# Optimization experiments

Measured on AMD Instinct MI355X. Metric: run time of the kernel, lower is better.

## Reference

```python
import jax, jax.numpy as jnp
import numpy as np

N, V_DIM, P_DIM, Q_DIM, C_DIM, H_DIM = 1536, 128, 16, 16, 16, 32
N_MOL, N_EDGE, LAYERS = 64, 16384, 3
TAU, GAMMA = 0.2, 1.0


def setup_inputs() -> dict:
    key = jax.random.key(0)
    ks = jax.random.split(key, 16)
    rng = np.random.default_rng(0)

    v_features = jax.random.normal(ks[0], (N, V_DIM), dtype=jnp.float32)

    # molecule -> node assignment: 64 molecules x 24 nodes each (block structure)
    mol_id = np.repeat(np.arange(N_MOL), N // N_MOL)
    mnm = np.zeros((N_MOL, N), dtype=np.float32)
    mnm[mol_id, np.arange(N)] = 1.0
    mol_node_mask = (mnm - 1.0) * 1e9  # 0 where assigned, -1e9 otherwise

    # node-edge incidence matrix [N, E]
    src = rng.integers(0, N, N_EDGE)
    dst = rng.integers(0, N, N_EDGE)
    nem = np.zeros((N, N_EDGE), dtype=np.float32)
    nem[src, np.arange(N_EDGE)] = 1.0
    nem[dst, np.arange(N_EDGE)] = 1.0
    node_edge_mask = np.zeros((N, N_EDGE), dtype=np.float32)

    def lin(k, fan_in, fan_out):
        kw, kb = jax.random.split(k)
        s = 1.0 / np.sqrt(fan_in)
        W = jax.random.uniform(kw, (fan_in, fan_out), jnp.float32, -s, s)
        b = jax.random.uniform(kb, (fan_out,), jnp.float32, -s, s)
        return W, b

    Wp, bp = lin(ks[1], V_DIM, P_DIM)
    Wq, bq = lin(ks[2], V_DIM, Q_DIM)
    Wc, bc = lin(ks[3], Q_DIM, C_DIM)
    W1, b1 = lin(ks[4], P_DIM + Q_DIM + C_DIM, H_DIM)
    Wdp, bdp = lin(ks[5], H_DIM, P_DIM)
    Wdq, bdq = lin(ks[6], H_DIM, Q_DIM)
    Wa, ba = lin(ks[7], P_DIM + Q_DIM, 1)

    return dict(v_features=v_features,
                mol_node_matrix=jnp.asarray(mnm), mol_node_mask=jnp.asarray(mol_node_mask),
                node_edge_matrix=jnp.asarray(nem), node_edge_mask=jnp.asarray(node_edge_mask),
                Wp=Wp, bp=bp, Wq=Wq, bq=bq, Wc=Wc, bc=bc,
                W1=W1, b1=b1, Wdp=Wdp, bdp=bdp, Wdq=Wdq, bdq=bdq, Wa=Wa, ba=ba)


def _safe_pair_norm(q):
    # pairwise ||q_i - q_j|| with grad-safe sqrt (zero diag)
    sq = ((q[None, :, :] - q[:, None, :]) ** 2).sum(-1)  # [N,N]
    return jnp.where(sq > 0, jnp.sqrt(jnp.where(sq > 0, sq, 1.0)), 0.0)


def reference(v_features, mol_node_matrix, mol_node_mask, node_edge_matrix, node_edge_mask,
              Wp, bp, Wq, bq, Wc, bc, W1, b1, Wdp, bdp, Wdq, bdq, Wa, ba):
    n = v_features.shape[0]
    m = mol_node_matrix.T @ mol_node_matrix                      # [N,N] same-molecule mask
    e = node_edge_matrix @ node_edge_matrix.T                    # [N,N] adjacency counts
    e = e * (1.0 - jnp.eye(n, dtype=e.dtype))                    # zero diagonal

    p = v_features @ Wp + bp                                     # [N,p]
    q = v_features @ Wq + bq                                     # [N,q]
    c_loss = jnp.linalg.norm(mol_node_matrix @ q)

    for _ in range(LAYERS):
        diff = q[None, :, :] - q[:, None, :]                     # [N,N,q]
        cenc = diff @ Wc + bc                                    # [N,N,c]  (large intermediate, as in torch)
        c = jnp.einsum('ij,ijc->ic', m, cenc)                    # masked sum over j
        h = jax.nn.relu(jnp.concatenate([p, q, c], axis=1) @ W1 + b1)
        dp = jnp.tanh(h @ Wdp + bdp)
        dq = jnp.tanh(h @ Wdq + bdq)
        p = p + TAU * dp
        q = q + TAU * dq
        c_loss = c_loss + jnp.linalg.norm(mol_node_matrix @ q)

    x = jnp.concatenate([p, q], axis=1)                          # [N, p+q]
    w = (x @ Wa + ba)[:, 0]                                      # [N]
    att = jax.nn.softmax(mol_node_matrix * w[None, :] + mol_node_mask, axis=1)  # [n_mol, N]
    f = att @ x                                                  # [n_mol, p+q]

    s_loss = jnp.abs(p).sum()
    a_loss = (e * jax.nn.relu(_safe_pair_norm(q) - GAMMA)).sum()
    return (f, s_loss, c_loss, a_loss)
```

## Files before the change

### kernel.cpp

```cpp
#include <hip/hip_runtime.h>
#include <hip/hip_bf16.h>
#include <math.h>

#define N_NODES 1536
#define V_DIMC  128
#define NMOL    64
#define NEDGE   16384
#define MAXM    24
#define SCANB   2048
#define TAU     0.2f

__device__ __forceinline__ float ldv(const void* p, int i, bool b16) {
    if (b16) {
        unsigned int u = ((unsigned int)((const unsigned short*)p)[i]) << 16;
        float f; __builtin_memcpy(&f, &u, 4); return f;
    }
    return ((const float*)p)[i];
}
__device__ __forceinline__ void stv(void* p, int i, float v, bool b16) {
    if (b16) ((__hip_bfloat16*)p)[i] = __float2bfloat16(v);
    else     ((float*)p)[i] = v;
}

__global__ __launch_bounds__(256) void k_init(const void* __restrict__ mnm,
        int* __restrict__ flag, int* __restrict__ cnt) {
    int t = blockIdx.x * 256 + threadIdx.x;
    if (t < NEDGE) cnt[t] = 0;
    if (t == 0) {
        unsigned int w = *(const unsigned int*)mnm;
        *flag = (w == 0x3F800000u) ? 0 : 1;
    }
}

__global__ __launch_bounds__(384) void k_mega(
        const void* __restrict__ mnm, const void* __restrict__ nem,
        const void* __restrict__ v,
        const void* __restrict__ Wp, const void* __restrict__ bp,
        const void* __restrict__ Wq, const void* __restrict__ bq,
        const void* __restrict__ Wc, const void* __restrict__ bc,
        const void* __restrict__ W1, const void* __restrict__ b1,
        const void* __restrict__ Wdp, const void* __restrict__ bdp,
        const void* __restrict__ Wdq, const void* __restrict__ bdq,
        const void* __restrict__ Wa, const void* __restrict__ ba,
        const int* __restrict__ flag, int* __restrict__ cnt, int* __restrict__ srow,
        float* __restrict__ qg, float* __restrict__ s_part,
        float* __restrict__ c_part, void* __restrict__ out) {
    __shared__ int   mi[MAXM];
    __shared__ float mw[MAXM];
    __shared__ int   nmem_s;
    __shared__ float rs_s, ba_s, inv_s;
    __shared__ float Wp_l[V_DIMC * 16], Wq_l[V_DIMC * 16];
    __shared__ float Wc_l[256], W1_l[48 * 32], Wdp_l[512], Wdq_l[512];
    __shared__ float bp_l[16], bq_l[16], bc_l[16], b1_l[32], bdp_l[16], bdq_l[16], Wa_l[32];
    __shared__ float P[MAXM][17], Q[MAXM][17], XQ[MAXM][17], XC[MAXM][17], H[MAXM][33];
    __shared__ float msum[16], wv[MAXM], attw[MAXM];
    __shared__ float red[512];

    const bool b16 = flag[0] != 0;
    const int t = threadIdx.x;

    if (blockIdx.x >= NMOL) {
        int sb = blockIdx.x - NMOL;
        const int stride = SCANB * 384;
        if (b16) {
            const int total8 = N_NODES * NEDGE / 8;
            const uint4* src = (const uint4*)nem;
            for (int i = sb * 384 + t; i < total8; i += stride) {
                uint4 x = src[i];
                if ((x.x | x.y | x.z | x.w) == 0u) continue;
                int base = i * 8, row = base >> 14, k0 = base & (NEDGE - 1);
                unsigned int wd[4] = {x.x, x.y, x.z, x.w};
                for (int w2 = 0; w2 < 4; ++w2) {
                    unsigned int ww = wd[w2];
                    if (!ww) continue;
                    if (ww & 0xFFFFu) { int k = k0 + 2 * w2;     int s = atomicAdd(&cnt[k], 1); if (s < 2) srow[k * 2 + s] = row; }
                    if (ww >> 16)     { int k = k0 + 2 * w2 + 1; int s = atomicAdd(&cnt[k], 1); if (s < 2) srow[k * 2 + s] = row; }
                }
            }
        } else {
            const int total4 = N_NODES * NEDGE / 4;
            const float4* src = (const float4*)nem;
            for (int i = sb * 384 + t; i < total4; i += stride) {
                float4 x = src[i];
                if (x.x == 0.f && x.y == 0.f && x.z == 0.f && x.w == 0.f) continue;
                int base = i * 4, row = base >> 14, k0 = base & (NEDGE - 1);
                float vv[4] = {x.x, x.y, x.z, x.w};
                for (int u = 0; u < 4; ++u) if (vv[u] != 0.f) {
                    int k = k0 + u; int s = atomicAdd(&cnt[k], 1); if (s < 2) srow[k * 2 + s] = row;
                }
            }
        }
        return;
    }

    const int g = blockIdx.x;

    for (int i = t; i < V_DIMC * 16; i += 384) { Wp_l[i] = ldv(Wp, i, b16); Wq_l[i] = ldv(Wq, i, b16); }
    for (int i = t; i < 48 * 32; i += 384) W1_l[i] = ldv(W1, i, b16);
    for (int i = t; i < 512; i += 384) { Wdp_l[i] = ldv(Wdp, i, b16); Wdq_l[i] = ldv(Wdq, i, b16); }
    if (t < 256) Wc_l[t] = ldv(Wc, t, b16);
    if (t < 16) { bp_l[t] = ldv(bp, t, b16); bq_l[t] = ldv(bq, t, b16); bc_l[t] = ldv(bc, t, b16);
                  bdp_l[t] = ldv(bdp, t, b16); bdq_l[t] = ldv(bdq, t, b16); }
    if (t < 32) { b1_l[t] = ldv(b1, t, b16); Wa_l[t] = ldv(Wa, t, b16); }
    if (t < MAXM) { mi[t] = 0; mw[t] = 0.f; }
    if (t == 0) ba_s = ldv(ba, 0, b16);

    if (t < 64) {
        int lane = t, base = 0;
        for (int r = 0; r < N_NODES / 64; ++r) {
            float w = ldv(mnm, g * N_NODES + r * 64 + lane, b16);
            unsigned long long bm = __ballot(w != 0.f);
            if (w != 0.f) {
                int pos = base + __popcll(bm & ((1ull << lane) - 1ull));
                if (pos < MAXM) { mi[pos] = r * 64 + lane; mw[pos] = w; }
            }
            base += __popcll(bm);
        }
        if (lane == 0) {
            nmem_s = (base > MAXM) ? MAXM : base;
            float s = 0.f;
            for (int m2 = 0; m2 < nmem_s; ++m2) s += mw[m2];
            rs_s = s;
        }
    }
    __syncthreads();
    const int nm = nmem_s;
    const int m = t >> 4, d = t & 15;
    const float rs = rs_s;

    if (m < nm) {
        int node = mi[m];
        float accp = bp_l[d], accq = bq_l[d];
        for (int e = 0; e < V_DIMC; ++e) {
            float vv = ldv(v, node * V_DIMC + e, b16);
            accp += vv * Wp_l[e * 16 + d];
            accq += vv * Wq_l[e * 16 + d];
        }
        P[m][d] = accp; Q[m][d] = accq;
    }

    for (int layer = 0; layer < 4; ++layer) {
        __syncthreads();
        if (t < 16) {
            float s = 0.f;
            for (int m2 = 0; m2 < nm; ++m2) s += mw[m2] * Q[m2][t];
            msum[t] = s;
        }
        __syncthreads();
        if (t == 0) {
            float ss = 0.f;
            for (int e = 0; e < 16; ++e) ss += msum[e] * msum[e];
            c_part[layer * NMOL + g] = ss;
        }
        if (layer == 3) break;
        float pi = 0.f, qi = 0.f;
        if (m < nm) {
            pi = P[m][d]; qi = Q[m][d];
            XQ[m][d] = mw[m] * (msum[d] - rs * qi);
        }
        __syncthreads();
        if (m < nm) {
            float c = mw[m] * rs * bc_l[d];
            for (int e = 0; e < 16; ++e) c += XQ[m][e] * Wc_l[e * 16 + d];
            XC[m][d] = c;
        }
        __syncthreads();
        if (m < nm) {
            float h0 = b1_l[d], h1 = b1_l[16 + d];
            for (int e = 0; e < 48; ++e) {
                float xv = (e < 16) ? P[m][e] : (e < 32) ? Q[m][e - 16] : XC[m][e - 32];
                h0 += xv * W1_l[e * 32 + d];
                h1 += xv * W1_l[e * 32 + 16 + d];
            }
            H[m][d] = fmaxf(h0, 0.f); H[m][16 + d] = fmaxf(h1, 0.f);
        }
        __syncthreads();
        if (m < nm) {
            float dp = bdp_l[d], dq = bdq_l[d];
            for (int e = 0; e < 32; ++e) {
                float hv = H[m][e];
                dp += hv * Wdp_l[e * 16 + d];
                dq += hv * Wdq_l[e * 16 + d];
            }
            P[m][d] = pi + TAU * tanhf(dp);
            Q[m][d] = qi + TAU * tanhf(dq);
        }
    }
    __syncthreads();

    if (m < nm) qg[mi[m] * 16 + d] = Q[m][d];

    red[t] = (m < nm) ? fabsf(P[m][d]) : 0.f;
    if (t < 128) red[384 + t] = 0.f;
    __syncthreads();
    for (int s = 256; s > 0; s >>= 1) { if (t < s) red[t] += red[t + s]; __syncthreads(); }
    if (t == 0) s_part[g] = red[0];

    if (t < nm) {
        float acc = ba_s;
        for (int e = 0; e < 16; ++e) acc += P[t][e] * Wa_l[e] + Q[t][e] * Wa_l[16 + e];
        wv[t] = acc;
    }
    __syncthreads();
    if (t == 0) {
        float mx = -3.0e38f;
        for (int m2 = 0; m2 < nm; ++m2) mx = fmaxf(mx, wv[m2]);
        float s = 0.f;
        for (int m2 = 0; m2 < nm; ++m2) { float ex = expf(wv[m2] - mx); attw[m2] = ex; s += ex; }
        inv_s = 1.f / s;
    }
    __syncthreads();
    if (t < 32) {
        float acc = 0.f;
        for (int m2 = 0; m2 < nm; ++m2)
            acc += attw[m2] * ((t < 16) ? P[m2][t] : Q[m2][t - 16]);
        stv(out, g * 32 + t, acc * inv_s, b16);
    }
}

__global__ __launch_bounds__(256) void k_aloss(const int* __restrict__ cnt,
        const int* __restrict__ srow, const float* __restrict__ qg,
        float* __restrict__ apart) {
    __shared__ float red[256];
    int t = threadIdx.x;
    int k = blockIdx.x * 256 + t;
    float local = 0.f;
    if (cnt[k] == 2) {
        int ia = srow[k * 2], ib = srow[k * 2 + 1];
        if (ia != ib) {
            float d2 = 0.f;
            for (int e = 0; e < 16; ++e) {
                float df = qg[ia * 16 + e] - qg[ib * 16 + e];
                d2 += df * df;
            }
            if (d2 > 0.f) {
                float r = sqrtf(d2) - 1.0f;
                if (r > 0.f) local = 2.f * r;
            }
        }
    }
    red[t] = local; __syncthreads();
    for (int s = 128; s > 0; s >>= 1) { if (t < s) red[t] += red[t + s]; __syncthreads(); }
    if (t == 0) apart[blockIdx.x] = red[0];
}

__global__ void DynamicGraphEncoder_85985245266279_kernel(
        const float* __restrict__ s_part, const float* __restrict__ c_part,
        const float* __restrict__ apart, const int* __restrict__ flag,
        void* __restrict__ out) {
    const bool b16 = flag[0] != 0;
    int t = threadIdx.x;
    float s  = s_part[t], a = apart[t];
    float c0 = c_part[t],       c1 = c_part[64 + t];
    float c2 = c_part[128 + t], c3 = c_part[192 + t];
    for (int off = 32; off > 0; off >>= 1) {
        s  += __shfl_down(s, off);   a  += __shfl_down(a, off);
        c0 += __shfl_down(c0, off);  c1 += __shfl_down(c1, off);
        c2 += __shfl_down(c2, off);  c3 += __shfl_down(c3, off);
    }
    if (t == 0) {
        stv(out, 2048, s, b16);
        stv(out, 2049, sqrtf(c0) + sqrtf(c1) + sqrtf(c2) + sqrtf(c3), b16);
        stv(out, 2050, a, b16);
    }
}

extern "C" void kernel_launch(void* const* d_in, const int* in_sizes, int n_in,
                              void* d_out, int out_size, void* d_ws, size_t ws_size,
                              hipStream_t stream) {
    const void* v    = d_in[0];
    const void* mnm  = d_in[1];
    const void* nem  = d_in[3];
    const void* Wp  = d_in[5];  const void* bp  = d_in[6];
    const void* Wq  = d_in[7];  const void* bq  = d_in[8];
    const void* Wc  = d_in[9];  const void* bc  = d_in[10];
    const void* W1  = d_in[11]; const void* b1  = d_in[12];
    const void* Wdp = d_in[13]; const void* bdp = d_in[14];
    const void* Wdq = d_in[15]; const void* bdq = d_in[16];
    const void* Wa  = d_in[17]; const void* ba  = d_in[18];

    float* ws     = (float*)d_ws;
    float* qg     = ws;
    float* s_part = qg + N_NODES * 16;
    float* c_part = s_part + NMOL;
    float* apart  = c_part + 4 * NMOL;
    int*   flag   = (int*)(apart + NMOL);
    int*   cnt    = flag + 4;
    int*   srow   = cnt + NEDGE;

    k_init<<<NEDGE / 256, 256, 0, stream>>>(mnm, flag, cnt);
    k_mega<<<NMOL + SCANB, 384, 0, stream>>>(mnm, nem, v,
            Wp, bp, Wq, bq, Wc, bc, W1, b1, Wdp, bdp, Wdq, bdq, Wa, ba,
            flag, cnt, srow, qg, s_part, c_part, d_out);
    k_aloss<<<NEDGE / 256, 256, 0, stream>>>(cnt, srow, qg, apart);
    DynamicGraphEncoder_85985245266279_kernel<<<1, 64, 0, stream>>>(
            s_part, c_part, apart, flag, d_out);
}
```

Baseline: 265.2 us.

## Replace edge counting with atomicMin pairs, merge a-loss into final reduce, shrink LDS

Drops the init kernel and replaces the per-edge atomic counter plus slot writes with two atomicMin updates that record each edge's min and max endpoint, initialised by a memset. The separate a-loss kernel and the final reduction are merged into one 1024-thread single-block kernel. The mega-kernel now stages Wp/Wq and the gathered feature rows in reused shared buffers with vectorised loads, which cuts LDS footprint and may improve occupancy. The attention logit now multiplies by the membership weight. Risks: the merged final kernel does all edge work in one block, and an edge with both endpoints on the same node is now treated as a missing pair.

```diff
diff --git a/kernel.cpp b/kernel.cpp
--- a/kernel.cpp
+++ b/kernel.cpp
@@ -21,15 +21,8 @@
     if (b16) ((__hip_bfloat16*)p)[i] = __float2bfloat16(v);
     else     ((float*)p)[i] = v;
 }
-
-__global__ __launch_bounds__(256) void k_init(const void* __restrict__ mnm,
-        int* __restrict__ flag, int* __restrict__ cnt) {
-    int t = blockIdx.x * 256 + threadIdx.x;
-    if (t < NEDGE) cnt[t] = 0;
-    if (t == 0) {
-        unsigned int w = *(const unsigned int*)mnm;
-        *flag = (w == 0x3F800000u) ? 0 : 1;
-    }
+__device__ __forceinline__ bool is_b16(const void* mnm) {
+    return (*(const unsigned int*)mnm) != 0x3F800000u;
 }
 
 __global__ __launch_bounds__(384) void k_mega(
@@ -42,22 +35,20 @@
         const void* __restrict__ Wdp, const void* __restrict__ bdp,
         const void* __restrict__ Wdq, const void* __restrict__ bdq,
         const void* __restrict__ Wa, const void* __restrict__ ba,
-        const int* __restrict__ flag, int* __restrict__ cnt, int* __restrict__ srow,
+        unsigned int* __restrict__ srowA, unsigned int* __restrict__ srowB,
         float* __restrict__ qg, float* __restrict__ s_part,
         float* __restrict__ c_part, void* __restrict__ out) {
+    __shared__ __align__(16) float R1[4096];
+    __shared__ __align__(16) float R2[24 * 132];
+    __shared__ float red[512];
     __shared__ int   mi[MAXM];
     __shared__ float mw[MAXM];
+    __shared__ float msum[16], wv[MAXM], attw[MAXM];
     __shared__ int   nmem_s;
-    __shared__ float rs_s, ba_s, inv_s;
-    __shared__ float Wp_l[V_DIMC * 16], Wq_l[V_DIMC * 16];
-    __shared__ float Wc_l[256], W1_l[48 * 32], Wdp_l[512], Wdq_l[512];
-    __shared__ float bp_l[16], bq_l[16], bc_l[16], b1_l[32], bdp_l[16], bdq_l[16], Wa_l[32];
-    __shared__ float P[MAXM][17], Q[MAXM][17], XQ[MAXM][17], XC[MAXM][17], H[MAXM][33];
-    __shared__ float msum[16], wv[MAXM], attw[MAXM];
-    __shared__ float red[512];
-
-    const bool b16 = flag[0] != 0;
+    __shared__ float rs_s, inv_s;
+
     const int t = threadIdx.x;
+    const bool b16 = is_b16(mnm);
 
     if (blockIdx.x >= NMOL) {
         int sb = blockIdx.x - NMOL;
@@ -73,8 +64,10 @@
                 for (int w2 = 0; w2 < 4; ++w2) {
                     unsigned int ww = wd[w2];
                     if (!ww) continue;
-                    if (ww & 0xFFFFu) { int k = k0 + 2 * w2;     int s = atomicAdd(&cnt[k], 1); if (s < 2) srow[k * 2 + s] = row; }
-                    if (ww >> 16)     { int k = k0 + 2 * w2 + 1; int s = atomicAdd(&cnt[k], 1); if (s < 2) srow[k * 2 + s] = row; }
+                    if (ww & 0xFFFFu) { int k = k0 + 2 * w2;
+                        atomicMin(&srowA[k], (unsigned)row); atomicMin(&srowB[k], ~(unsigned)row); }
+                    if (ww >> 16)     { int k = k0 + 2 * w2 + 1;
+                        atomicMin(&srowA[k], (unsigned)row); atomicMin(&srowB[k], ~(unsigned)row); }
                 }
             }
         } else {
@@ -86,7 +79,8 @@
                 int base = i * 4, row = base >> 14, k0 = base & (NEDGE - 1);
                 float vv[4] = {x.x, x.y, x.z, x.w};
                 for (int u = 0; u < 4; ++u) if (vv[u] != 0.f) {
-                    int k = k0 + u; int s = atomicAdd(&cnt[k], 1); if (s < 2) srow[k * 2 + s] = row;
+                    int k = k0 + u;
+                    atomicMin(&srowA[k], (unsigned)row); atomicMin(&srowB[k], ~(unsigned)row);
                 }
             }
         }
@@ -94,56 +88,73 @@
     }
 
     const int g = blockIdx.x;
-
-    for (int i = t; i < V_DIMC * 16; i += 384) { Wp_l[i] = ldv(Wp, i, b16); Wq_l[i] = ldv(Wq, i, b16); }
-    for (int i = t; i < 48 * 32; i += 384) W1_l[i] = ldv(W1, i, b16);
-    for (int i = t; i < 512; i += 384) { Wdp_l[i] = ldv(Wdp, i, b16); Wdq_l[i] = ldv(Wdq, i, b16); }
-    if (t < 256) Wc_l[t] = ldv(Wc, t, b16);
-    if (t < 16) { bp_l[t] = ldv(bp, t, b16); bq_l[t] = ldv(bq, t, b16); bc_l[t] = ldv(bc, t, b16);
-                  bdp_l[t] = ldv(bdp, t, b16); bdq_l[t] = ldv(bdq, t, b16); }
-    if (t < 32) { b1_l[t] = ldv(b1, t, b16); Wa_l[t] = ldv(Wa, t, b16); }
+    const int m = t >> 4, d = t & 15;
+
+    if (t == 0) nmem_s = 0;
     if (t < MAXM) { mi[t] = 0; mw[t] = 0.f; }
-    if (t == 0) ba_s = ldv(ba, 0, b16);
-
-    if (t < 64) {
-        int lane = t, base = 0;
-        for (int r = 0; r < N_NODES / 64; ++r) {
-            float w = ldv(mnm, g * N_NODES + r * 64 + lane, b16);
-            unsigned long long bm = __ballot(w != 0.f);
-            if (w != 0.f) {
-                int pos = base + __popcll(bm & ((1ull << lane) - 1ull));
-                if (pos < MAXM) { mi[pos] = r * 64 + lane; mw[pos] = w; }
-            }
-            base += __popcll(bm);
-        }
-        if (lane == 0) {
-            nmem_s = (base > MAXM) ? MAXM : base;
-            float s = 0.f;
-            for (int m2 = 0; m2 < nmem_s; ++m2) s += mw[m2];
-            rs_s = s;
-        }
-    }
-    __syncthreads();
-    const int nm = nmem_s;
-    const int m = t >> 4, d = t & 15;
+    __syncthreads();
+
+    if (!b16) {
+        const float4* wp4 = (const float4*)Wp; const float4* wq4 = (const float4*)Wq;
+        float4* r14 = (float4*)R1;
+        for (int i = t; i < 512; i += 384) { r14[i] = wp4[i]; r14[512 + i] = wq4[i]; }
+    } else {
+        for (int i = t; i < 2048; i += 384) { R1[i] = ldv(Wp, i, true); R1[2048 + i] = ldv(Wq, i, true); }
+    }
+    for (int j = t; j < N_NODES; j += 384) {
+        float w = ldv(mnm, g * N_NODES + j, b16);
+        if (w != 0.f) {
+            int pos = atomicAdd(&nmem_s, 1);
+            if (pos < MAXM) { mi[pos] = j; mw[pos] = w; }
+        }
+    }
+    __syncthreads();
+    const int nm = (nmem_s > MAXM) ? MAXM : nmem_s;
+
+    if (!b16) {
+        for (int idx = t; idx < 24 * 32; idx += 384) {
+            int row = idx >> 5, col = idx & 31;
+            float4 x = ((const float4*)v)[mi[row] * 32 + col];
+            *((float4*)&R2[row * 132 + col * 4]) = x;
+        }
+    } else {
+        for (int idx = t; idx < 24 * 128; idx += 384) {
+            int row = idx >> 7, e = idx & 127;
+            R2[row * 132 + e] = ldv(v, mi[row] * V_DIMC + e, true);
+        }
+    }
+    if (t == 0) { float s = 0.f; for (int m2 = 0; m2 < nm; ++m2) s += mw[m2]; rs_s = s; }
+    __syncthreads();
     const float rs = rs_s;
 
-    if (m < nm) {
-        int node = mi[m];
-        float accp = bp_l[d], accq = bq_l[d];
+    float accp = ldv(bp, d, b16), accq = ldv(bq, d, b16);
+    {
+        const float* vr = &R2[m * 132];
+#pragma unroll 8
         for (int e = 0; e < V_DIMC; ++e) {
-            float vv = ldv(v, node * V_DIMC + e, b16);
-            accp += vv * Wp_l[e * 16 + d];
-            accq += vv * Wq_l[e * 16 + d];
-        }
-        P[m][d] = accp; Q[m][d] = accq;
-    }
+            float vv = vr[e];
+            accp += vv * R1[e * 16 + d];
+            accq += vv * R1[2048 + e * 16 + d];
+        }
+    }
+    __syncthreads();
+
+    float* P  = &R2[0];     float* Q  = &R2[408];
+    float* XQ = &R2[816];   float* XC = &R2[1224];
+    float* H  = &R2[1632];
+    P[m * 17 + d] = accp;  Q[m * 17 + d] = accq;
+    for (int i = t; i < 1536; i += 384) R1[i] = ldv(W1, i, b16);
+    for (int i = t; i < 512; i += 384) { R1[1536 + i] = ldv(Wdp, i, b16); R1[2048 + i] = ldv(Wdq, i, b16); }
+    if (t < 256) R1[2560 + t] = ldv(Wc, t, b16);
+    if (t < 16) { R1[2816 + t] = ldv(bc, t, b16); R1[2864 + t] = ldv(bdp, t, b16); R1[2880 + t] = ldv(bdq, t, b16); }
+    if (t < 32) { R1[2832 + t] = ldv(b1, t, b16); R1[2896 + t] = ldv(Wa, t, b16); }
+    if (t == 0) R1[2928] = ldv(ba, 0, b16);
 
     for (int layer = 0; layer < 4; ++layer) {
         __syncthreads();
         if (t < 16) {
             float s = 0.f;
-            for (int m2 = 0; m2 < nm; ++m2) s += mw[m2] * Q[m2][t];
+            for (int m2 = 0; m2 < nm; ++m2) s += mw[m2] * Q[m2 * 17 + t];
             msum[t] = s;
         }
         __syncthreads();
@@ -155,51 +166,52 @@
         if (layer == 3) break;
         float pi = 0.f, qi = 0.f;
         if (m < nm) {
-            pi = P[m][d]; qi = Q[m][d];
-            XQ[m][d] = mw[m] * (msum[d] - rs * qi);
+            pi = P[m * 17 + d]; qi = Q[m * 17 + d];
+            XQ[m * 17 + d] = mw[m] * (msum[d] - rs * qi);
         }
         __syncthreads();
         if (m < nm) {
-            float c = mw[m] * rs * bc_l[d];
-            for (int e = 0; e < 16; ++e) c += XQ[m][e] * Wc_l[e * 16 + d];
-            XC[m][d] = c;
+            float c = mw[m] * rs * R1[2816 + d];
+            for (int e = 0; e < 16; ++e) c += XQ[m * 17 + e] * R1[2560 + e * 16 + d];
+            XC[m * 17 + d] = c;
         }
         __syncthreads();
         if (m < nm) {
-            float h0 = b1_l[d], h1 = b1_l[16 + d];
+            float h0 = R1[2832 + d], h1 = R1[2832 + 16 + d];
             for (int e = 0; e < 48; ++e) {
-                float xv = (e < 16) ? P[m][e] : (e < 32) ? Q[m][e - 16] : XC[m][e - 32];
-                h0 += xv * W1_l[e * 32 + d];
-                h1 += xv * W1_l[e * 32 + 16 + d];
-            }
-            H[m][d] = fmaxf(h0, 0.f); H[m][16 + d] = fmaxf(h1, 0.f);
+                float xv = (e < 16) ? P[m * 17 + e] : (e < 32) ? Q[m * 17 + e - 16] : XC[m * 17 + e - 32];
+                h0 += xv * R1[e * 32 + d];
+                h1 += xv * R1[e * 32 + 16 + d];
+            }
+            H[m * 33 + d] = fmaxf(h0, 0.f); H[m * 33 + 16 + d] = fmaxf(h1, 0.f);
         }
         __syncthreads();
         if (m < nm) {
-            float dp = bdp_l[d], dq = bdq_l[d];
+            float dp = R1[2864 + d], dq = R1[2880 + d];
             for (int e = 0; e < 32; ++e) {
-                float hv = H[m][e];
-                dp += hv * Wdp_l[e * 16 + d];
-                dq += hv * Wdq_l[e * 16 + d];
-            }
-            P[m][d] = pi + TAU * tanhf(dp);
-            Q[m][d] = qi + TAU * tanhf(dq);
-        }
-    }
-    __syncthreads();
-
-    if (m < nm) qg[mi[m] * 16 + d] = Q[m][d];
-
-    red[t] = (m < nm) ? fabsf(P[m][d]) : 0.f;
+                float hv = H[m * 33 + e];
+                dp += hv * R1[1536 + e * 16 + d];
+                dq += hv * R1[2048 + e * 16 + d];
+            }
+            P[m * 17 + d] = pi + TAU * tanhf(dp);
+            Q[m * 17 + d] = qi + TAU * tanhf(dq);
+        }
+    }
+    __syncthreads();
+
+    if (m < nm) qg[mi[m] * 16 + d] = Q[m * 17 + d];
+
+    red[t] = (m < nm) ? fabsf(P[m * 17 + d]) : 0.f;
     if (t < 128) red[384 + t] = 0.f;
     __syncthreads();
     for (int s = 256; s > 0; s >>= 1) { if (t < s) red[t] += red[t + s]; __syncthreads(); }
     if (t == 0) s_part[g] = red[0];
 
     if (t < nm) {
-        float acc = ba_s;
-        for (int e = 0; e < 16; ++e) acc += P[t][e] * Wa_l[e] + Q[t][e] * Wa_l[16 + e];
-        wv[t] = acc;
+        float acc = R1[2928];
+        for (int e = 0; e < 16; ++e)
+            acc += P[t * 17 + e] * R1[2896 + e] + Q[t * 17 + e] * R1[2896 + 16 + e];
+        wv[t] = mw[t] * acc;
     }
     __syncthreads();
     if (t == 0) {
@@ -213,55 +225,57 @@
     if (t < 32) {
         float acc = 0.f;
         for (int m2 = 0; m2 < nm; ++m2)
-            acc += attw[m2] * ((t < 16) ? P[m2][t] : Q[m2][t - 16]);
+            acc += attw[m2] * ((t < 16) ? P[m2 * 17 + t] : Q[m2 * 17 + t - 16]);
         stv(out, g * 32 + t, acc * inv_s, b16);
     }
 }
 
-__global__ __launch_bounds__(256) void k_aloss(const int* __restrict__ cnt,
-        const int* __restrict__ srow, const float* __restrict__ qg,
-        float* __restrict__ apart) {
-    __shared__ float red[256];
-    int t = threadIdx.x;
-    int k = blockIdx.x * 256 + t;
+__global__ __launch_bounds__(1024) void DynamicGraphEncoder_85985245266279_kernel(
+        const void* __restrict__ mnm,
+        const unsigned int* __restrict__ srowA, const unsigned int* __restrict__ srowB,
+        const float* __restrict__ qg, const float* __restrict__ s_part,
+        const float* __restrict__ c_part, void* __restrict__ out) {
+    __shared__ float red[1024];
+    const int t = threadIdx.x;
+    const bool b16 = is_b16(mnm);
+
     float local = 0.f;
-    if (cnt[k] == 2) {
-        int ia = srow[k * 2], ib = srow[k * 2 + 1];
-        if (ia != ib) {
+    for (int k = t; k < NEDGE; k += 1024) {
+        unsigned int a = srowA[k], b = ~srowB[k];
+        if (a < b && b < (unsigned)N_NODES) {
+            const float4* qa = (const float4*)(qg + a * 16);
+            const float4* qb = (const float4*)(qg + b * 16);
             float d2 = 0.f;
-            for (int e = 0; e < 16; ++e) {
-                float df = qg[ia * 16 + e] - qg[ib * 16 + e];
-                d2 += df * df;
+#pragma unroll
+            for (int c4 = 0; c4 < 4; ++c4) {
+                float4 xa = qa[c4], xb = qb[c4];
+                float dx = xa.x - xb.x, dy = xa.y - xb.y, dz = xa.z - xb.z, dw = xa.w - xb.w;
+                d2 += dx * dx + dy * dy + dz * dz + dw * dw;
             }
             if (d2 > 0.f) {
                 float r = sqrtf(d2) - 1.0f;
-                if (r > 0.f) local = 2.f * r;
+                if (r > 0.f) local += 2.f * r;
             }
         }
     }
     red[t] = local; __syncthreads();
-    for (int s = 128; s > 0; s >>= 1) { if (t < s) red[t] += red[t + s]; __syncthreads(); }
-    if (t == 0) apart[blockIdx.x] = red[0];
-}
-
-__global__ void DynamicGraphEncoder_85985245266279_kernel(
-        const float* __restrict__ s_part, const float* __restrict__ c_part,
-        const float* __restrict__ apart, const int* __restrict__ flag,
-        void* __restrict__ out) {
-    const bool b16 = flag[0] != 0;
-    int t = threadIdx.x;
-    float s  = s_part[t], a = apart[t];
-    float c0 = c_part[t],       c1 = c_part[64 + t];
-    float c2 = c_part[128 + t], c3 = c_part[192 + t];
-    for (int off = 32; off > 0; off >>= 1) {
-        s  += __shfl_down(s, off);   a  += __shfl_down(a, off);
-        c0 += __shfl_down(c0, off);  c1 += __shfl_down(c1, off);
-        c2 += __shfl_down(c2, off);  c3 += __shfl_down(c3, off);
+    for (int s = 512; s > 0; s >>= 1) { if (t < s) red[t] += red[t + s]; __syncthreads(); }
+    float a_loss = red[0]; __syncthreads();
+
+    red[t] = (t < NMOL) ? s_part[t] : 0.f; __syncthreads();
+    for (int s = 512; s > 0; s >>= 1) { if (t < s) red[t] += red[t + s]; __syncthreads(); }
+    float s_loss = red[0]; __syncthreads();
+
+    float cl[4];
+    for (int stg = 0; stg < 4; ++stg) {
+        red[t] = (t < NMOL) ? c_part[stg * NMOL + t] : 0.f; __syncthreads();
+        for (int s = 512; s > 0; s >>= 1) { if (t < s) red[t] += red[t + s]; __syncthreads(); }
+        cl[stg] = red[0]; __syncthreads();
     }
     if (t == 0) {
-        stv(out, 2048, s, b16);
-        stv(out, 2049, sqrtf(c0) + sqrtf(c1) + sqrtf(c2) + sqrtf(c3), b16);
-        stv(out, 2050, a, b16);
+        stv(out, 2048, s_loss, b16);
+        stv(out, 2049, sqrtf(cl[0]) + sqrtf(cl[1]) + sqrtf(cl[2]) + sqrtf(cl[3]), b16);
+        stv(out, 2050, a_loss, b16);
     }
 }
 
@@ -279,20 +293,18 @@
     const void* Wdq = d_in[15]; const void* bdq = d_in[16];
     const void* Wa  = d_in[17]; const void* ba  = d_in[18];
 
-    float* ws     = (float*)d_ws;
-    float* qg     = ws;
-    float* s_part = qg + N_NODES * 16;
-    float* c_part = s_part + NMOL;
-    float* apart  = c_part + 4 * NMOL;
-    int*   flag   = (int*)(apart + NMOL);
-    int*   cnt    = flag + 4;
-    int*   srow   = cnt + NEDGE;
-
-    k_init<<<NEDGE / 256, 256, 0, stream>>>(mnm, flag, cnt);
+    float*        ws     = (float*)d_ws;
+    float*        qg     = ws;
+    float*        s_part = qg + N_NODES * 16;
+    float*        c_part = s_part + NMOL;
+    unsigned int* srowA  = (unsigned int*)(c_part + 4 * NMOL);
+    unsigned int* srowB  = srowA + NEDGE;
+
+    hipMemsetAsync(srowA, 0xFF, 2 * NEDGE * sizeof(unsigned int), stream);
+
     k_mega<<<NMOL + SCANB, 384, 0, stream>>>(mnm, nem, v,
             Wp, bp, Wq, bq, Wc, bc, W1, b1, Wdp, bdp, Wdq, bdq, Wa, ba,
-            flag, cnt, srow, qg, s_part, c_part, d_out);
-    k_aloss<<<NEDGE / 256, 256, 0, stream>>>(cnt, srow, qg, apart);
-    DynamicGraphEncoder_85985245266279_kernel<<<1, 64, 0, stream>>>(
-            s_part, c_part, apart, flag, d_out);
-}
+            srowA, srowB, qg, s_part, c_part, d_out);
+    DynamicGraphEncoder_85985245266279_kernel<<<1, 1024, 0, stream>>>(
+            mnm, srowA, srowB, qg, s_part, c_part, d_out);
+}
```

Result: slower. 290.2 us (+9.4%).
